# Optimization experiments

Measured on AMD Instinct MI355X. Metric: run time of the kernel, lower is better.

## Reference

```python
import jax, jax.numpy as jnp
import numpy as np

DIM = 128

def _mlp2(x, W1, b1, W2, b2):
    return jax.nn.relu(x @ W1 + b1) @ W2 + b2

def setup_inputs() -> dict:
    key = jax.random.key(0)
    ks = jax.random.split(key, 16)
    n_var, n_con, n_nodes = 600000, 400000, 1000000
    s2 = 1.0 / np.sqrt(2.0)
    sd = 1.0 / np.sqrt(DIM)
    inp = {
        'var_node_features': jax.random.normal(ks[0], (n_var, 2), jnp.float32),
        'con_node_features': jax.random.normal(ks[1], (n_con, 2), jnp.float32),
        'node_types': jnp.zeros((n_nodes,), jnp.int32),
        'assoc_var': jnp.arange(n_var, dtype=jnp.int64),
        'assoc_con': jnp.arange(n_con, dtype=jnp.int64),
        # var_mlp params
        'vW1': jax.random.uniform(ks[2], (2, DIM), jnp.float32, -s2, s2),
        'vb1': jnp.zeros((DIM,), jnp.float32),
        'vW2': jax.random.uniform(ks[3], (DIM, DIM), jnp.float32, -sd, sd),
        'vb2': jnp.zeros((DIM,), jnp.float32),
        # con_mlp params
        'cW1': jax.random.uniform(ks[4], (2, DIM), jnp.float32, -s2, s2),
        'cb1': jnp.zeros((DIM,), jnp.float32),
        'cW2': jax.random.uniform(ks[5], (DIM, DIM), jnp.float32, -sd, sd),
        'cb2': jnp.zeros((DIM,), jnp.float32),
        # head params fc1..fc4
        'W1': jax.random.uniform(ks[6], (DIM, DIM), jnp.float32, -sd, sd),
        'b1': jnp.zeros((DIM,), jnp.float32),
        'W2': jax.random.uniform(ks[7], (DIM, DIM), jnp.float32, -sd, sd),
        'b2': jnp.zeros((DIM,), jnp.float32),
        'W3': jax.random.uniform(ks[8], (DIM, DIM), jnp.float32, -sd, sd),
        'b3': jnp.zeros((DIM,), jnp.float32),
        'W4': jax.random.uniform(ks[9], (DIM, 1), jnp.float32, -sd, sd),
        'b4': jnp.zeros((1,), jnp.float32),
    }
    return inp

def reference(var_node_features, con_node_features, node_types, assoc_var, assoc_con,
              vW1, vb1, vW2, vb2, cW1, cb1, cW2, cb2,
              W1, b1, W2, b2, W3, b3, W4, b4):
    n = _mlp2(var_node_features, vW1, vb1, vW2, vb2)   # [n_var, dim]
    e = _mlp2(con_node_features, cW1, cb1, cW2, cb2)   # [n_con, dim]
    # scatter into shared node tensor (var first, then con overwrites)
    x = jnp.zeros((node_types.shape[0], n.shape[-1]), n.dtype)
    x = x.at[assoc_var].set(n)
    x = x.at[assoc_con].set(e)
    # gather variable-node embeddings
    x = x[assoc_var]                                   # [n_var, dim]
    x = jax.nn.relu(x @ W1 + b1)  # dropout is identity in eval mode
    x = jax.nn.relu(x @ W2 + b2)
    x = jax.nn.relu(x @ W3 + b3)
    x = jax.nn.sigmoid(x @ W4 + b4)
    return x.squeeze(-1)
```

## Files before the change

### kernel.cpp

```cpp
#include <hip/hip_runtime.h>
#include <hip/hip_bf16.h>

typedef unsigned short u16;
typedef unsigned int u32;
typedef __attribute__((ext_vector_type(8))) short short8;
typedef __attribute__((ext_vector_type(4))) float f32x4;

#define MFMA16(a, b, c) __builtin_amdgcn_mfma_f32_16x16x32_bf16((a), (b), (c), 0, 0, 0)

__device__ __forceinline__ u32 pack2(float a, float b) {
    union { __hip_bfloat162 h; u32 u; } v;
    v.h = __float22bfloat162_rn(make_float2(a, b));
    return v.u;
}
__device__ __forceinline__ u16 f2b(float f) {
    union { float f; u32 i; } v; v.f = f;
    u32 x = v.i;
    return (u16)((x + 0x7FFFu + ((x >> 16) & 1u)) >> 16);
}

__global__ void wt_prep(const float* __restrict__ vW2, const float* __restrict__ cW2,
                        const float* __restrict__ W1f, const float* __restrict__ W2f,
                        const float* __restrict__ W3f, u16* __restrict__ wt) {
    int i = blockIdx.x * 256 + threadIdx.x;
    if (i >= 5 * 16384) return;
    int l = i >> 14, e = i & 16383;
    int fr = e >> 9, lane = (e >> 3) & 63, j = e & 7;
    int ot = fr >> 2, ks = fr & 3;
    int c = lane & 15, q = lane >> 4;
    int f = 32 * ks + 16 * (j >> 2) + 4 * q + (j & 3);
    const float* src = (l == 0) ? vW2 : (l == 1) ? cW2 : (l == 2) ? W1f
                     : (l == 3) ? W2f : W3f;
    wt[i] = f2b(src[f * 128 + ot * 16 + c]);
}

#define PRE_H(WL, BSRC, H) do {                                                \
    _Pragma("unroll")                                                          \
    for (int fr = 0; fr < 16; ++fr)                                            \
        wf[fr].s = *(const short8*)((WL) + ((H) * 16 + fr) * 512 + lane * 8);  \
    _Pragma("unroll")                                                          \
    for (int o = 0; o < 4; ++o)                                                \
        biv[o] = *(const float4*)((BSRC) + ((H) * 4 + o) * 16 + q * 4);        \
} while (0)

#define HALF_MID(BIN, BOUT, H, RELU) do {                                      \
    _Pragma("unroll")                                                          \
    for (int o = 0; o < 4; ++o) {                                              \
        const int ot = (H) * 4 + o;                                            \
        _Pragma("unroll")                                                      \
        for (int rt = 0; rt < 4; ++rt) {                                       \
            f32x4 acc = {biv[o].x, biv[o].y, biv[o].z, biv[o].w};              \
            acc = MFMA16(wf[o * 4 + 0].s, BIN[rt][0].s, acc);                  \
            acc = MFMA16(wf[o * 4 + 1].s, BIN[rt][1].s, acc);                  \
            acc = MFMA16(wf[o * 4 + 2].s, BIN[rt][2].s, acc);                  \
            acc = MFMA16(wf[o * 4 + 3].s, BIN[rt][3].s, acc);                  \
            float v0 = acc[0], v1 = acc[1], v2 = acc[2], v3 = acc[3];          \
            if (RELU) {                                                        \
                v0 = fmaxf(v0, 0.f); v1 = fmaxf(v1, 0.f);                      \
                v2 = fmaxf(v2, 0.f); v3 = fmaxf(v3, 0.f);                      \
            }                                                                  \
            BOUT[rt][ot >> 1].u[2 * (ot & 1) + 0] = pack2(v0, v1);             \
            BOUT[rt][ot >> 1].u[2 * (ot & 1) + 1] = pack2(v2, v3);             \
        }                                                                      \
    }                                                                          \
} while (0)

#define HALF_LAST(BIN, H) do {                                                 \
    _Pragma("unroll")                                                          \
    for (int o = 0; o < 4; ++o) {                                              \
        const int ot = (H) * 4 + o;                                            \
        float4 ww = *(const float4*)(W4 + ot * 16 + q * 4);                    \
        _Pragma("unroll")                                                      \
        for (int rt = 0; rt < 4; ++rt) {                                       \
            f32x4 acc = {biv[o].x, biv[o].y, biv[o].z, biv[o].w};              \
            acc = MFMA16(wf[o * 4 + 0].s, BIN[rt][0].s, acc);                  \
            acc = MFMA16(wf[o * 4 + 1].s, BIN[rt][1].s, acc);                  \
            acc = MFMA16(wf[o * 4 + 2].s, BIN[rt][2].s, acc);                  \
            acc = MFMA16(wf[o * 4 + 3].s, BIN[rt][3].s, acc);                  \
            pd[rt] += fmaxf(acc[0], 0.f) * ww.x + fmaxf(acc[1], 0.f) * ww.y    \
                    + fmaxf(acc[2], 0.f) * ww.z + fmaxf(acc[3], 0.f) * ww.w;   \
        }                                                                      \
    }                                                                          \
} while (0)

__global__ void __launch_bounds__(128, 2) mlp_fused(
    const float* __restrict__ varf, const float* __restrict__ conf,
    const float* __restrict__ vW1, const float* __restrict__ vb1, const float* __restrict__ vb2,
    const float* __restrict__ cW1, const float* __restrict__ cb1, const float* __restrict__ cb2,
    const float* __restrict__ b1,  const float* __restrict__ b2,  const float* __restrict__ b3,
    const float* __restrict__ W4,  const float* __restrict__ b4,
    const u16* __restrict__ WT,   float* __restrict__ out,
    int n_var, int n_con)
{
    const int t = threadIdx.x;
    const int lane = t & 63, wv = t >> 6;
    const int c = lane & 15, q = lane >> 4;
    const int row0 = blockIdx.x * 128;
    const int rowW = row0 + wv * 64;
    const bool use_con = (row0 < n_con);

    union frag { u32 u[4]; short8 s; };
    frag bbA[4][4], bbB[4][4];
    frag wf[16];
    float4 biv[4];

    const u16* WL0 = WT + (size_t)16384 * (use_con ? 1 : 0);
    const u16* WL1 = WT + (size_t)16384 * 2;
    const u16* WL2 = WT + (size_t)16384 * 3;
    const u16* WL3 = WT + (size_t)16384 * 4;
    const float* bs0 = use_con ? cb2 : vb2;

    PRE_H(WL0, bs0, 0);

    {
        const float* w1p = use_con ? cW1 : vW1;
        const float* b1p = use_con ? cb1 : vb1;
        const float* fb  = use_con ? conf : varf;
        float in0[4], in1[4];
#pragma unroll
        for (int rt = 0; rt < 4; ++rt) {
            int g = rowW + rt * 16 + c;
            in0[rt] = 0.f; in1[rt] = 0.f;
            if (g < n_var) { float2 w = *(const float2*)(fb + 2 * g); in0[rt] = w.x; in1[rt] = w.y; }
        }
#pragma unroll
        for (int ks = 0; ks < 4; ++ks) {
#pragma unroll
            for (int hi = 0; hi < 2; ++hi) {
                int base = ks * 32 + hi * 16 + q * 4;
                float4 wA = *(const float4*)(w1p + base);
                float4 wB = *(const float4*)(w1p + 128 + base);
                float4 bz = *(const float4*)(b1p + base);
#pragma unroll
                for (int rt = 0; rt < 4; ++rt) {
                    float x0 = fmaxf(in0[rt] * wA.x + in1[rt] * wB.x + bz.x, 0.f);
                    float x1 = fmaxf(in0[rt] * wA.y + in1[rt] * wB.y + bz.y, 0.f);
                    float x2 = fmaxf(in0[rt] * wA.z + in1[rt] * wB.z + bz.z, 0.f);
                    float x3 = fmaxf(in0[rt] * wA.w + in1[rt] * wB.w + bz.w, 0.f);
                    bbA[rt][ks].u[2 * hi + 0] = pack2(x0, x1);
                    bbA[rt][ks].u[2 * hi + 1] = pack2(x2, x3);
                }
            }
        }
    }

    float pd[4] = {0.f, 0.f, 0.f, 0.f};

    HALF_MID(bbA, bbB, 0, 0);
    PRE_H(WL0, bs0, 1);  HALF_MID(bbA, bbB, 1, 0);
    PRE_H(WL1, b1, 0);   HALF_MID(bbB, bbA, 0, 1);
    PRE_H(WL1, b1, 1);   HALF_MID(bbB, bbA, 1, 1);
    PRE_H(WL2, b2, 0);   HALF_MID(bbA, bbB, 0, 1);
    PRE_H(WL2, b2, 1);   HALF_MID(bbA, bbB, 1, 1);
    PRE_H(WL3, b3, 0);   HALF_LAST(bbB, 0);
    PRE_H(WL3, b3, 1);   HALF_LAST(bbB, 1);

    float bias4 = b4[0];
#pragma unroll
    for (int rt = 0; rt < 4; ++rt) {
        float v = pd[rt];
        v += __shfl_xor(v, 16);
        v += __shfl_xor(v, 32);
        if (q == 0) {
            int g = rowW + rt * 16 + c;
            if (g < n_var) out[g] = 1.f / (1.f + __expf(-(v + bias4)));
        }
    }
}

extern "C" void kernel_launch(void* const* d_in, const int* in_sizes, int n_in,
                              void* d_out, int out_size, void* d_ws, size_t ws_size,
                              hipStream_t stream) {
    const float* varf = (const float*)d_in[0];
    const float* conf = (const float*)d_in[1];
    const float* vW1 = (const float*)d_in[5];
    const float* vb1 = (const float*)d_in[6];
    const float* vW2 = (const float*)d_in[7];
    const float* vb2 = (const float*)d_in[8];
    const float* cW1 = (const float*)d_in[9];
    const float* cb1 = (const float*)d_in[10];
    const float* cW2 = (const float*)d_in[11];
    const float* cb2 = (const float*)d_in[12];
    const float* W1  = (const float*)d_in[13];
    const float* b1  = (const float*)d_in[14];
    const float* W2  = (const float*)d_in[15];
    const float* b2  = (const float*)d_in[16];
    const float* W3  = (const float*)d_in[17];
    const float* b3  = (const float*)d_in[18];
    const float* W4  = (const float*)d_in[19];
    const float* b4  = (const float*)d_in[20];

    int n_var = in_sizes[0] / 2;
    int n_con = in_sizes[1] / 2;
    u16* wt = (u16*)d_ws;

    hipLaunchKernelGGL(wt_prep, dim3(320), dim3(256), 0, stream,
                       vW2, cW2, W1, W2, W3, wt);

    int nb = (n_var + 127) / 128;
    hipLaunchKernelGGL(mlp_fused, dim3(nb), dim3(128), 0, stream,
                       varf, conf, vW1, vb1, vb2, cW1, cb1, cb2,
                       b1, b2, b3, W4, b4, wt, (float*)d_out, n_var, n_con);
}
```

Measured before the change: 183.9 us.

## Switch fused MLP from 16x16x32 to 32x32x16 bf16 MFMA tiles

Recasts the whole fused MLP chain to use 32x32x16 MFMA instructions, with a new packed-weight layout in wt_prep, a new activation fragment layout, and a reworked first-layer and final reduction. Larger MFMA tiles mean fewer instructions and fewer weight-fragment loads per output, which should lift matrix-core throughput. Weights are now loaded per 32-column output block inside each layer rather than in staged halves. The catch is 16-wide accumulators, which raise register pressure and may cut occupancy or cause spills.

```diff
diff --git a/kernel.cpp b/kernel.cpp
--- a/kernel.cpp
+++ b/kernel.cpp
@@ -4,9 +4,9 @@
 typedef unsigned short u16;
 typedef unsigned int u32;
 typedef __attribute__((ext_vector_type(8))) short short8;
-typedef __attribute__((ext_vector_type(4))) float f32x4;
-
-#define MFMA16(a, b, c) __builtin_amdgcn_mfma_f32_16x16x32_bf16((a), (b), (c), 0, 0, 0)
+typedef __attribute__((ext_vector_type(16))) float f32x16;
+
+#define MFMA32(a, b, c) __builtin_amdgcn_mfma_f32_32x32x16_bf16((a), (b), (c), 0, 0, 0)
 
 __device__ __forceinline__ u32 pack2(float a, float b) {
     union { __hip_bfloat162 h; u32 u; } v;
@@ -26,59 +26,77 @@
     if (i >= 5 * 16384) return;
     int l = i >> 14, e = i & 16383;
     int fr = e >> 9, lane = (e >> 3) & 63, j = e & 7;
-    int ot = fr >> 2, ks = fr & 3;
-    int c = lane & 15, q = lane >> 4;
-    int f = 32 * ks + 16 * (j >> 2) + 4 * q + (j & 3);
+    int ot2 = fr >> 3, ks = fr & 7;
+    int lc = lane & 31, h = lane >> 5;
+    int f = 32 * (ks >> 1) + 16 * (ks & 1) + 8 * (j >> 2) + 4 * h + (j & 3);
     const float* src = (l == 0) ? vW2 : (l == 1) ? cW2 : (l == 2) ? W1f
                      : (l == 3) ? W2f : W3f;
-    wt[i] = f2b(src[f * 128 + ot * 16 + c]);
-}
-
-#define PRE_H(WL, BSRC, H) do {                                                \
+    wt[i] = f2b(src[f * 128 + ot2 * 32 + lc]);
+}
+
+#define LAYER_MID(BIN, BOUT, WL, BSRC, RELU) do {                              \
     _Pragma("unroll")                                                          \
-    for (int fr = 0; fr < 16; ++fr)                                            \
-        wf[fr].s = *(const short8*)((WL) + ((H) * 16 + fr) * 512 + lane * 8);  \
-    _Pragma("unroll")                                                          \
-    for (int o = 0; o < 4; ++o)                                                \
-        biv[o] = *(const float4*)((BSRC) + ((H) * 4 + o) * 16 + q * 4);        \
-} while (0)
-
-#define HALF_MID(BIN, BOUT, H, RELU) do {                                      \
-    _Pragma("unroll")                                                          \
-    for (int o = 0; o < 4; ++o) {                                              \
-        const int ot = (H) * 4 + o;                                            \
-        _Pragma("unroll")                                                      \
-        for (int rt = 0; rt < 4; ++rt) {                                       \
-            f32x4 acc = {biv[o].x, biv[o].y, biv[o].z, biv[o].w};              \
-            acc = MFMA16(wf[o * 4 + 0].s, BIN[rt][0].s, acc);                  \
-            acc = MFMA16(wf[o * 4 + 1].s, BIN[rt][1].s, acc);                  \
-            acc = MFMA16(wf[o * 4 + 2].s, BIN[rt][2].s, acc);                  \
-            acc = MFMA16(wf[o * 4 + 3].s, BIN[rt][3].s, acc);                  \
-            float v0 = acc[0], v1 = acc[1], v2 = acc[2], v3 = acc[3];          \
-            if (RELU) {                                                        \
-                v0 = fmaxf(v0, 0.f); v1 = fmaxf(v1, 0.f);                      \
-                v2 = fmaxf(v2, 0.f); v3 = fmaxf(v3, 0.f);                      \
+    for (int ot2 = 0; ot2 < 4; ++ot2) {                                        \
+        frag wa[8];                                                            \
+        _Pragma("unroll")                                                      \
+        for (int ks = 0; ks < 8; ++ks)                                         \
+            wa[ks].s = *(const short8*)((WL) + (ot2 * 8 + ks) * 512 + lane * 8);\
+        float4 bv0 = *(const float4*)((BSRC) + 32 * ot2 + 0  + 4 * h);         \
+        float4 bv1 = *(const float4*)((BSRC) + 32 * ot2 + 8  + 4 * h);         \
+        float4 bv2 = *(const float4*)((BSRC) + 32 * ot2 + 16 + 4 * h);         \
+        float4 bv3 = *(const float4*)((BSRC) + 32 * ot2 + 24 + 4 * h);         \
+        _Pragma("unroll")                                                      \
+        for (int rt2 = 0; rt2 < 2; ++rt2) {                                    \
+            f32x16 acc = {bv0.x, bv0.y, bv0.z, bv0.w, bv1.x, bv1.y, bv1.z,     \
+                          bv1.w, bv2.x, bv2.y, bv2.z, bv2.w, bv3.x, bv3.y,     \
+                          bv3.z, bv3.w};                   \
+            _Pragma("unroll")                                                  \
+            for (int ks = 0; ks < 8; ++ks)                                     \
+                acc = MFMA32(wa[ks].s, BIN[rt2][ks].s, acc);                   \
+            _Pragma("unroll")                                                  \
+            for (int s = 0; s < 2; ++s) {                                      \
+                _Pragma("unroll")                                              \
+                for (int p = 0; p < 4; ++p) {                                  \
+                    float ve = acc[8 * s + 2 * p], vo = acc[8 * s + 2 * p + 1];\
+                    if (RELU) { ve = fmaxf(ve, 0.f); vo = fmaxf(vo, 0.f); }    \
+                    BOUT[rt2][2 * ot2 + s].u[p] = pack2(ve, vo);               \
+                }                                                              \
             }                                                                  \
-            BOUT[rt][ot >> 1].u[2 * (ot & 1) + 0] = pack2(v0, v1);             \
-            BOUT[rt][ot >> 1].u[2 * (ot & 1) + 1] = pack2(v2, v3);             \
         }                                                                      \
     }                                                                          \
 } while (0)
 
-#define HALF_LAST(BIN, H) do {                                                 \
+#define LAYER_LAST(BIN, WL, BSRC) do {                                         \
     _Pragma("unroll")                                                          \
-    for (int o = 0; o < 4; ++o) {                                              \
-        const int ot = (H) * 4 + o;                                            \
-        float4 ww = *(const float4*)(W4 + ot * 16 + q * 4);                    \
-        _Pragma("unroll")                                                      \
-        for (int rt = 0; rt < 4; ++rt) {                                       \
-            f32x4 acc = {biv[o].x, biv[o].y, biv[o].z, biv[o].w};              \
-            acc = MFMA16(wf[o * 4 + 0].s, BIN[rt][0].s, acc);                  \
-            acc = MFMA16(wf[o * 4 + 1].s, BIN[rt][1].s, acc);                  \
-            acc = MFMA16(wf[o * 4 + 2].s, BIN[rt][2].s, acc);                  \
-            acc = MFMA16(wf[o * 4 + 3].s, BIN[rt][3].s, acc);                  \
-            pd[rt] += fmaxf(acc[0], 0.f) * ww.x + fmaxf(acc[1], 0.f) * ww.y    \
-                    + fmaxf(acc[2], 0.f) * ww.z + fmaxf(acc[3], 0.f) * ww.w;   \
+    for (int ot2 = 0; ot2 < 4; ++ot2) {                                        \
+        frag wa[8];                                                            \
+        _Pragma("unroll")                                                      \
+        for (int ks = 0; ks < 8; ++ks)                                         \
+            wa[ks].s = *(const short8*)((WL) + (ot2 * 8 + ks) * 512 + lane * 8);\
+        float4 bv0 = *(const float4*)((BSRC) + 32 * ot2 + 0  + 4 * h);         \
+        float4 bv1 = *(const float4*)((BSRC) + 32 * ot2 + 8  + 4 * h);         \
+        float4 bv2 = *(const float4*)((BSRC) + 32 * ot2 + 16 + 4 * h);         \
+        float4 bv3 = *(const float4*)((BSRC) + 32 * ot2 + 24 + 4 * h);         \
+        float4 ww0 = *(const float4*)(W4 + 32 * ot2 + 0  + 4 * h);             \
+        float4 ww1 = *(const float4*)(W4 + 32 * ot2 + 8  + 4 * h);             \
+        float4 ww2 = *(const float4*)(W4 + 32 * ot2 + 16 + 4 * h);             \
+        float4 ww3 = *(const float4*)(W4 + 32 * ot2 + 24 + 4 * h);             \
+        _Pragma("unroll")                                                      \
+        for (int rt2 = 0; rt2 < 2; ++rt2) {                                    \
+            f32x16 acc = {bv0.x, bv0.y, bv0.z, bv0.w, bv1.x, bv1.y, bv1.z,     \
+                          bv1.w, bv2.x, bv2.y, bv2.z, bv2.w, bv3.x, bv3.y,     \
+                          bv3.z, bv3.w};                                       \
+            _Pragma("unroll")                                                  \
+            for (int ks = 0; ks < 8; ++ks)                                     \
+                acc = MFMA32(wa[ks].s, BIN[rt2][ks].s, acc);                   \
+            pd[rt2] += fmaxf(acc[0],  0.f) * ww0.x + fmaxf(acc[1],  0.f) * ww0.y \
+                     + fmaxf(acc[2],  0.f) * ww0.z + fmaxf(acc[3],  0.f) * ww0.w \
+                     + fmaxf(acc[4],  0.f) * ww1.x + fmaxf(acc[5],  0.f) * ww1.y \
+                     + fmaxf(acc[6],  0.f) * ww1.z + fmaxf(acc[7],  0.f) * ww1.w \
+                     + fmaxf(acc[8],  0.f) * ww2.x + fmaxf(acc[9],  0.f) * ww2.y \
+                     + fmaxf(acc[10], 0.f) * ww2.z + fmaxf(acc[11], 0.f) * ww2.w \
+                     + fmaxf(acc[12], 0.f) * ww3.x + fmaxf(acc[13], 0.f) * ww3.y \
+                     + fmaxf(acc[14], 0.f) * ww3.z + fmaxf(acc[15], 0.f) * ww3.w;\
         }                                                                      \
     }                                                                          \
 } while (0)
@@ -94,15 +112,47 @@
 {
     const int t = threadIdx.x;
     const int lane = t & 63, wv = t >> 6;
-    const int c = lane & 15, q = lane >> 4;
+    const int lc = lane & 31, h = lane >> 5;
     const int row0 = blockIdx.x * 128;
     const int rowW = row0 + wv * 64;
     const bool use_con = (row0 < n_con);
 
     union frag { u32 u[4]; short8 s; };
-    frag bbA[4][4], bbB[4][4];
-    frag wf[16];
-    float4 biv[4];
+    frag bbA[2][8], bbB[2][8];
+
+    {
+        const float* w1p = use_con ? cW1 : vW1;
+        const float* b1p = use_con ? cb1 : vb1;
+        const float* fb  = use_con ? conf : varf;
+        float in0[2], in1[2];
+#pragma unroll
+        for (int rt2 = 0; rt2 < 2; ++rt2) {
+            int g = rowW + rt2 * 32 + lc;
+            in0[rt2] = 0.f; in1[rt2] = 0.f;
+            if (g < n_var) { float2 w = *(const float2*)(fb + 2 * g); in0[rt2] = w.x; in1[rt2] = w.y; }
+        }
+#pragma unroll
+        for (int ks = 0; ks < 8; ++ks) {
+#pragma unroll
+            for (int pp = 0; pp < 2; ++pp) {
+                int base = 32 * (ks >> 1) + 16 * (ks & 1) + 8 * pp + 4 * h;
+                float4 wA = *(const float4*)(w1p + base);
+                float4 wB = *(const float4*)(w1p + 128 + base);
+                float4 bz = *(const float4*)(b1p + base);
+#pragma unroll
+                for (int rt2 = 0; rt2 < 2; ++rt2) {
+                    float x0 = fmaxf(in0[rt2] * wA.x + in1[rt2] * wB.x + bz.x, 0.f);
+                    float x1 = fmaxf(in0[rt2] * wA.y + in1[rt2] * wB.y + bz.y, 0.f);
+                    float x2 = fmaxf(in0[rt2] * wA.z + in1[rt2] * wB.z + bz.z, 0.f);
+                    float x3 = fmaxf(in0[rt2] * wA.w + in1[rt2] * wB.w + bz.w, 0.f);
+                    bbA[rt2][ks].u[2 * pp + 0] = pack2(x0, x1);
+                    bbA[rt2][ks].u[2 * pp + 1] = pack2(x2, x3);
+                }
+            }
+        }
+    }
+
+    float pd[2] = {0.f, 0.f};
 
     const u16* WL0 = WT + (size_t)16384 * (use_con ? 1 : 0);
     const u16* WL1 = WT + (size_t)16384 * 2;
@@ -110,59 +160,18 @@
     const u16* WL3 = WT + (size_t)16384 * 4;
     const float* bs0 = use_con ? cb2 : vb2;
 
-    PRE_H(WL0, bs0, 0);
-
-    {
-        const float* w1p = use_con ? cW1 : vW1;
-        const float* b1p = use_con ? cb1 : vb1;
-        const float* fb  = use_con ? conf : varf;
-        float in0[4], in1[4];
-#pragma unroll
-        for (int rt = 0; rt < 4; ++rt) {
-            int g = rowW + rt * 16 + c;
-            in0[rt] = 0.f; in1[rt] = 0.f;
-            if (g < n_var) { float2 w = *(const float2*)(fb + 2 * g); in0[rt] = w.x; in1[rt] = w.y; }
-        }
-#pragma unroll
-        for (int ks = 0; ks < 4; ++ks) {
-#pragma unroll
-            for (int hi = 0; hi < 2; ++hi) {
-                int base = ks * 32 + hi * 16 + q * 4;
-                float4 wA = *(const float4*)(w1p + base);
-                float4 wB = *(const float4*)(w1p + 128 + base);
-                float4 bz = *(const float4*)(b1p + base);
-#pragma unroll
-                for (int rt = 0; rt < 4; ++rt) {
-                    float x0 = fmaxf(in0[rt] * wA.x + in1[rt] * wB.x + bz.x, 0.f);
-                    float x1 = fmaxf(in0[rt] * wA.y + in1[rt] * wB.y + bz.y, 0.f);
-                    float x2 = fmaxf(in0[rt] * wA.z + in1[rt] * wB.z + bz.z, 0.f);
-                    float x3 = fmaxf(in0[rt] * wA.w + in1[rt] * wB.w + bz.w, 0.f);
-                    bbA[rt][ks].u[2 * hi + 0] = pack2(x0, x1);
-                    bbA[rt][ks].u[2 * hi + 1] = pack2(x2, x3);
-                }
-            }
-        }
-    }
-
-    float pd[4] = {0.f, 0.f, 0.f, 0.f};
-
-    HALF_MID(bbA, bbB, 0, 0);
-    PRE_H(WL0, bs0, 1);  HALF_MID(bbA, bbB, 1, 0);
-    PRE_H(WL1, b1, 0);   HALF_MID(bbB, bbA, 0, 1);
-    PRE_H(WL1, b1, 1);   HALF_MID(bbB, bbA, 1, 1);
-    PRE_H(WL2, b2, 0);   HALF_MID(bbA, bbB, 0, 1);
-    PRE_H(WL2, b2, 1);   HALF_MID(bbA, bbB, 1, 1);
-    PRE_H(WL3, b3, 0);   HALF_LAST(bbB, 0);
-    PRE_H(WL3, b3, 1);   HALF_LAST(bbB, 1);
+    LAYER_MID(bbA, bbB, WL0, bs0, 0);
+    LAYER_MID(bbB, bbA, WL1, b1, 1);
+    LAYER_MID(bbA, bbB, WL2, b2, 1);
+    LAYER_LAST(bbB, WL3, b3);
 
     float bias4 = b4[0];
 #pragma unroll
-    for (int rt = 0; rt < 4; ++rt) {
-        float v = pd[rt];
-        v += __shfl_xor(v, 16);
+    for (int rt2 = 0; rt2 < 2; ++rt2) {
+        float v = pd[rt2];
         v += __shfl_xor(v, 32);
-        if (q == 0) {
-            int g = rowW + rt * 16 + c;
+        if (h == 0) {
+            int g = rowW + rt2 * 32 + lc;
             if (g < n_var) out[g] = 1.f / (1.f + __expf(-(v + bias4)));
         }
     }
```

After: 187.5 us. No clear change (+2.0%).
